# Kernel tuning notes

Measured on AMD Instinct MI355X. Metric: run time of the kernel, lower is better.

The kernel has to match this reference:

```python
import jax, jax.numpy as jnp
import numpy as np

N_EMBD = 1024
N_HEAD = 16
SEQ_LEN = 2048
BATCH = 4
ROPE_THETA = 10000.0


def _rope_tables(T, hd, dtype=jnp.float32):
    freqs = 1.0 / (ROPE_THETA ** (jnp.arange(0, hd, 2, dtype=jnp.float32) / hd))
    t = jnp.arange(T, dtype=jnp.float32)
    ang = jnp.outer(t, freqs)  # [T, hd//2]
    return jnp.cos(ang).astype(dtype), jnp.sin(ang).astype(dtype)


def _apply_rope(x, cos, sin):
    # x: [B,H,T,hd]; cos/sin: [T, hd//2]
    hd = x.shape[-1]
    x1, x2 = x[..., : hd // 2], x[..., hd // 2 :]
    c = cos[None, None, : x.shape[2], :]
    s = sin[None, None, : x.shape[2], :]
    return jnp.concatenate([x1 * c - x2 * s, x2 * c + x1 * s], axis=-1)


def _rms_norm(x):
    eps = jnp.finfo(x.dtype).eps
    return x * jax.lax.rsqrt(jnp.mean(jnp.square(x), axis=-1, keepdims=True) + eps)


def setup_inputs() -> dict:
    key = jax.random.key(0)
    k1, k2, k3, k4 = jax.random.split(key, 4)
    C = N_EMBD
    x = jax.random.normal(k1, (BATCH, SEQ_LEN, C), dtype=jnp.float32)
    w_attn = jax.random.normal(k2, (C, 3 * C), dtype=jnp.float32) * (1.0 / np.sqrt(C))
    w_proj = jax.random.normal(k3, (C, C), dtype=jnp.float32) * (1.0 / np.sqrt(C))
    val_embed = jax.random.normal(k4, (SEQ_LEN, C), dtype=jnp.float32) * 0.02
    return {"x": x, "w_attn": w_attn, "w_proj": w_proj, "val_embed": val_embed}


def reference(x, w_attn, w_proj, val_embed):
    B, T, C = x.shape
    H = N_HEAD
    hd = C // H

    qkv = x @ w_attn  # [B,T,3C]
    q, k, v = jnp.split(qkv, 3, axis=-1)
    v = v + val_embed[:T]

    def to_heads(t):
        return t.reshape(B, T, H, hd).transpose(0, 2, 1, 3)  # [B,H,T,hd]

    q, k, v = to_heads(q), to_heads(k), to_heads(v)

    cos, sin = _rope_tables(T, hd, x.dtype)
    q = _rms_norm(_apply_rope(q, cos, sin))
    k = _rms_norm(_apply_rope(k, cos, sin))

    scale = 1.0 / np.sqrt(hd)
    scores = jnp.einsum("bhqd,bhkd->bhqk", q, k) * scale  # [B,H,T,T]
    causal = jnp.tril(jnp.ones((T, T), dtype=bool))
    scores = jnp.where(causal[None, None], scores, jnp.finfo(scores.dtype).min)
    attn = jax.nn.softmax(scores, axis=-1)
    y = jnp.einsum("bhqk,bhkd->bhqd", attn, v)  # [B,H,T,hd]
    y = y.transpose(0, 2, 1, 3).reshape(B, T, C)
    return y @ w_proj
```

## Files before the change

kernel.cpp:

```cpp
#include <hip/hip_runtime.h>
#include <float.h>
#include <math.h>

#define BB 4
#define TT 2048
#define CC 1024
#define HH 16
#define HD 64
#define C3 3072

typedef __bf16 bf16;
typedef __bf16 bf16x8 __attribute__((ext_vector_type(8)));
typedef __bf16 bf16x4 __attribute__((ext_vector_type(4)));
typedef float f32x4 __attribute__((ext_vector_type(4)));
typedef float f32x16 __attribute__((ext_vector_type(16)));
typedef unsigned int uint32x4 __attribute__((ext_vector_type(4)));

#define QSCALE 0.18033688f

__device__ __forceinline__ void gload16(const void* g, void* l) {
    __builtin_amdgcn_global_load_lds(
        (const __attribute__((address_space(1))) void*)g,
        (__attribute__((address_space(3))) void*)l, 16, 0, 0);
}

__global__ __launch_bounds__(256) void rope_table_k(float* __restrict__ tab) {
    int idx = blockIdx.x * 256 + threadIdx.x;
    if (idx >= TT * 32) return;
    int t = idx >> 5;
    int j = idx & 31;
    float freq = powf(10000.0f, -((float)(2 * j)) / 64.0f);
    float ang = (float)t * freq;
    tab[idx] = cosf(ang);
    tab[TT * 32 + idx] = sinf(ang);
}

__global__ __launch_bounds__(256) void cvt_f2b_k(const float* __restrict__ in,
                                                 bf16* __restrict__ out, int n8) {
    int i = blockIdx.x * 256 + threadIdx.x;
    if (i >= n8) return;
    const float4* p = (const float4*)(in + (size_t)i * 8);
    float4 a = p[0], b = p[1];
    bf16x8 o;
    o[0] = (bf16)a.x; o[1] = (bf16)a.y; o[2] = (bf16)a.z; o[3] = (bf16)a.w;
    o[4] = (bf16)b.x; o[5] = (bf16)b.y; o[6] = (bf16)b.z; o[7] = (bf16)b.w;
    *(bf16x8*)(out + (size_t)i * 8) = o;
}

__global__ __launch_bounds__(256) void transW_k(const float* __restrict__ in,
                                                bf16* __restrict__ out, int K, int N) {
    __shared__ bf16 tile[64][72];
    int n0 = blockIdx.x * 64, k0 = blockIdx.y * 64;
    int t = threadIdx.x;
    int r = t >> 2, c4 = (t & 3) * 16;
    const float4* src = (const float4*)(in + (size_t)(k0 + r) * N + n0 + c4);
    #pragma unroll
    for (int j = 0; j < 4; ++j) {
        float4 v = src[j];
        tile[r][c4 + 4 * j + 0] = (bf16)v.x; tile[r][c4 + 4 * j + 1] = (bf16)v.y;
        tile[r][c4 + 4 * j + 2] = (bf16)v.z; tile[r][c4 + 4 * j + 3] = (bf16)v.w;
    }
    __syncthreads();
    bf16x8 o0, o1;
    #pragma unroll
    for (int j = 0; j < 8; ++j) o0[j] = tile[c4 + j][r];
    #pragma unroll
    for (int j = 0; j < 8; ++j) o1[j] = tile[c4 + 8 + j][r];
    *(bf16x8*)(out + (size_t)(n0 + r) * K + k0 + c4) = o0;
    *(bf16x8*)(out + (size_t)(n0 + r) * K + k0 + c4 + 8) = o1;
}

__global__ __launch_bounds__(512, 1) void gemm256_k(const bf16* __restrict__ A,
                                                    const bf16* __restrict__ BT,
                                                    bf16* __restrict__ Qh,
                                                    bf16* __restrict__ Kh,
                                                    bf16* __restrict__ Vh,
                                                    int M, int N, int K) {
    extern __shared__ bf16 smem[];
    const int tid = threadIdx.x;
    const int w = tid >> 6, lane = tid & 63;
    const int wm = w >> 2, wn = w & 3;
    const int nwg = (int)gridDim.x;
    const int cpx = nwg >> 3;
    const int flat = (int)blockIdx.x;
    const int wg = (flat & 7) * cpx + (flat >> 3);
    const int gx = N / 192;
    const int n0 = (wg % gx) * 192;
    const int m0 = (wg / gx) * 256;

    const int srow = lane >> 3;
    const int schunk = (lane & 7) ^ srow;
    const int xorL = (lane & 7) << 3;
    const int KT = K >> 6;

    const bf16* Bb = BT + (size_t)(n0 + wn * 48 + (lane & 15)) * K + (lane >> 4) * 8;

    f32x4 acc[8][3];
    #pragma unroll
    for (int i = 0; i < 8; ++i)
        #pragma unroll
        for (int j = 0; j < 3; ++j) acc[i][j] = {0.f, 0.f, 0.f, 0.f};

    auto stageA = [&](int kt, bf16* Abuf) {
        const int k0 = kt * 64;
        #pragma unroll
        for (int ri = 0; ri < 4; ++ri) {
            int row = ri * 64 + w * 8;
            gload16(A + (size_t)(m0 + row + srow) * K + k0 + schunk * 8,
                    Abuf + row * 64);
        }
    };

    stageA(0, smem);
    __syncthreads();

    for (int kt = 0; kt < KT; ++kt) {
        const int buf = kt & 1;
        if (kt + 1 < KT) stageA(kt + 1, smem + (buf ^ 1) * 16384);
        const bf16* Al = smem + buf * 16384;
        #pragma unroll
        for (int kh = 0; kh < 2; ++kh) {
            const int off = (kh * 32 + (lane >> 4) * 8) ^ xorL;
            bf16x8 aF[8], bF[3];
            #pragma unroll
            for (int j = 0; j < 3; ++j)
                bF[j] = *(const bf16x8*)(Bb + (size_t)(j * 16) * K + kt * 64 + kh * 32);
            #pragma unroll
            for (int i = 0; i < 8; ++i)
                aF[i] = *(const bf16x8*)&Al[(wm * 128 + i * 16 + (lane & 15)) * 64 + off];
            __builtin_amdgcn_s_setprio(1);
            #pragma unroll
            for (int i = 0; i < 8; ++i)
                #pragma unroll
                for (int j = 0; j < 3; ++j)
                    acc[i][j] = __builtin_amdgcn_mfma_f32_16x16x32_bf16(
                        aF[i], bF[j], acc[i][j], 0, 0, 0);
            __builtin_amdgcn_s_setprio(0);
        }
        __syncthreads();
    }

    const int ncb = n0 + wn * 48;
    #pragma unroll
    for (int j = 0; j < 3; ++j) {
        const int ncbj = ncb + j * 16;
        const int region = ncbj >> 10;
        const int hj = (ncbj & 1023) >> 6;
        const int cj = (ncbj & 63) + (lane & 15);
        bf16* dst = (region == 0) ? Qh : ((region == 1) ? Kh : Vh);
        #pragma unroll
        for (int i = 0; i < 8; ++i)
            #pragma unroll
            for (int r = 0; r < 4; ++r) {
                int m = m0 + wm * 128 + i * 16 + 4 * (lane >> 4) + r;
                int b = m >> 11, t = m & (TT - 1);
                dst[((size_t)(b * HH + hj) * TT + t) * HD + cj] = (bf16)acc[i][j][r];
            }
    }
}

__global__ __launch_bounds__(256) void gemm_bt_k(const bf16* __restrict__ A,
                                                 const bf16* __restrict__ BT,
                                                 float* __restrict__ C,
                                                 int M, int N, int K) {
    __shared__ bf16 Al[128 * 64];
    __shared__ bf16 Bl[128 * 64];
    const int tid = threadIdx.x;
    const int w = tid >> 6, lane = tid & 63;
    const int flat = (int)blockIdx.x;
    const int xcd = flat & 7;
    const int local = flat >> 3;
    const int lr = local >> 3, lc = local & 7;
    const int m0 = (xcd * 8 + lr) * 128;
    const int n0 = lc * 128;
    const int wrow = (w >> 1) * 64, wcol = (w & 1) * 64;
    const int srow = lane >> 3;
    const int selem = (((lane & 7) ^ srow) << 3);
    const int xorL = (lane & 7) << 3;

    const f32x4 fz = {0.f, 0.f, 0.f, 0.f};
    f32x4 acc[4][4];
    #pragma unroll
    for (int i = 0; i < 4; ++i)
        #pragma unroll
        for (int j = 0; j < 4; ++j) acc[i][j] = fz;

    for (int k0 = 0; k0 < K; k0 += 64) {
        __syncthreads();
        #pragma unroll
        for (int jj = 0; jj < 4; ++jj) {
            int c = w * 4 + jj;
            int row = c * 8 + srow;
            gload16(A + (size_t)(m0 + row) * K + k0 + selem, &Al[c * 512]);
            gload16(BT + (size_t)(n0 + row) * K + k0 + selem, &Bl[c * 512]);
        }
        __syncthreads();
        #pragma unroll
        for (int kh = 0; kh < 2; ++kh) {
            const int off = (kh * 32 + (lane >> 4) * 8) ^ xorL;
            bf16x8 aF[4], bF[4];
            #pragma unroll
            for (int i = 0; i < 4; ++i) {
                aF[i] = *(const bf16x8*)&Al[(wrow + i * 16 + (lane & 15)) * 64 + off];
                bF[i] = *(const bf16x8*)&Bl[(wcol + i * 16 + (lane & 15)) * 64 + off];
            }
            #pragma unroll
            for (int i = 0; i < 4; ++i)
                #pragma unroll
                for (int j = 0; j < 4; ++j)
                    acc[i][j] = __builtin_amdgcn_mfma_f32_16x16x32_bf16(
                        aF[i], bF[j], acc[i][j], 0, 0, 0);
        }
    }

    #pragma unroll
    for (int i = 0; i < 4; ++i)
        #pragma unroll
        for (int r = 0; r < 4; ++r) {
            size_t rowm = (size_t)(m0 + wrow + i * 16 + 4 * (lane >> 4) + r);
            #pragma unroll
            for (int j = 0; j < 4; ++j)
                C[rowm * N + n0 + wcol + j * 16 + (lane & 15)] = acc[i][j][r];
        }
}

__global__ __launch_bounds__(256) void rope_rms_k(bf16* __restrict__ Qh,
                                                  bf16* __restrict__ Kh,
                                                  const bf16* __restrict__ Vh,
                                                  bf16* __restrict__ Vt,
                                                  const float* __restrict__ emb,
                                                  const float* __restrict__ tab) {
    __shared__ bf16 tile[64][72];
    const int t0 = blockIdx.x * 64;
    const int bh = blockIdx.y;
    const int h = bh & (HH - 1);
    const int w = threadIdx.x >> 6, lane = threadIdx.x & 63;
    const int j = lane & 31;
    #pragma unroll 4
    for (int i = 0; i < 16; ++i) {
        const int tl = w * 16 + i;
        const int t = t0 + tl;
        const size_t base = ((size_t)bh * TT + t) * HD + lane;
        const float cs = tab[t * 32 + j];
        const float sn = tab[TT * 32 + t * 32 + j];
        float q = (float)Qh[base], k = (float)Kh[base], v = (float)Vh[base];
        float qp = __shfl_xor(q, 32, 64), kp = __shfl_xor(k, 32, 64);
        float rq = (lane < 32) ? q * cs - qp * sn : q * cs + qp * sn;
        float rk = (lane < 32) ? k * cs - kp * sn : k * cs + kp * sn;
        float sq = rq * rq, sk = rk * rk;
        #pragma unroll
        for (int off = 1; off < 64; off <<= 1) {
            sq += __shfl_xor(sq, off, 64);
            sk += __shfl_xor(sk, off, 64);
        }
        rq *= rsqrtf(sq * (1.0f / 64.0f) + 1.1920929e-07f);
        rk *= rsqrtf(sk * (1.0f / 64.0f) + 1.1920929e-07f);
        Qh[base] = (bf16)(rq * QSCALE);
        Kh[base] = (bf16)rk;
        tile[tl][lane] = (bf16)(v + emb[(size_t)t * CC + h * HD + lane]);
    }
    __syncthreads();
    const int tt = threadIdx.x;
    const int r = tt >> 2, c4 = (tt & 3) * 16;
    bf16x8 o0, o1;
    #pragma unroll
    for (int jj = 0; jj < 8; ++jj) o0[jj] = tile[c4 + jj][r];
    #pragma unroll
    for (int jj = 0; jj < 8; ++jj) o1[jj] = tile[c4 + 8 + jj][r];
    bf16* out = Vt + (size_t)bh * HD * TT;
    *(bf16x8*)(out + (size_t)r * TT + t0 + c4) = o0;
    *(bf16x8*)(out + (size_t)r * TT + t0 + c4 + 8) = o1;
}

__global__ __launch_bounds__(512) void attn_k(const bf16* __restrict__ Qh,
                                              const bf16* __restrict__ Kh,
                                              const bf16* __restrict__ Vt,
                                              bf16* __restrict__ Y) {
    extern __shared__ bf16 asmem[];
    bf16* KlB = asmem;
    bf16* VlB = asmem + 16384;
    const int flat = (int)blockIdx.y * 8 + (int)blockIdx.x;
    const int slot = flat >> 3;
    const int bh = (flat & 7) * 8 + (slot & 7);
    const int u = slot >> 3;
    const int qb = (u < 4) ? (7 - u) : (u - 4);
    const int b = bh >> 4, h = bh & 15;
    const int tid = threadIdx.x, w = tid >> 6, lane = tid & 63;
    const int hi = lane >> 5, q31 = lane & 31;
    const int wq0 = qb * 256 + w * 32;
    const int qg = wq0 + q31;
    const int xr = q31 & 7;

    const bf16* Kbase = Kh + (size_t)bh * TT * HD;
    const bf16* Vbase = Vt + (size_t)bh * HD * TT;

    bf16x8 qF[4];
    {
        const bf16* qp = Qh + (size_t)bh * TT * HD + (size_t)qg * HD + hi * 8;
        #pragma unroll
        for (int ds = 0; ds < 4; ++ds) qF[ds] = *(const bf16x8*)(qp + ds * 16);
    }

    f32x16 accY[2];
    #pragma unroll
    for (int i = 0; i < 16; ++i) { accY[0][i] = 0.f; accY[1][i] = 0.f; }
    float mR = -INFINITY, lR = 0.f;

    const int srow = lane >> 3;
    const int schunk = (lane & 7) ^ srow;
    const int vsr = lane >> 4;
    const int ktN = 2 * qb + 2;

    auto stageKV = [&](int kt, int buf) {
        const int kc0 = kt * 128;
        #pragma unroll
        for (int jj = 0; jj < 2; ++jj) {
            int lr = w * 16 + jj * 8;
            gload16(Kbase + (size_t)(kc0 + lr + srow) * HD + schunk * 8,
                    KlB + buf * 8192 + lr * 64);
            int vr = w * 8 + jj * 4;
            int vrow = vr + vsr;
            gload16(Vbase + (size_t)vrow * TT + kc0 + (((lane & 15) ^ (vrow & 7)) * 8),
                    VlB + buf * 8192 + vr * 128);
        }
    };

    stageKV(0, 0);
    asm volatile("s_waitcnt vmcnt(0)" ::: "memory");
    __builtin_amdgcn_s_barrier();
    __builtin_amdgcn_sched_barrier(0);

    for (int kt = 0; kt < ktN; ++kt) {
        const int buf = kt & 1;
        if (kt + 1 < ktN) stageKV(kt + 1, buf ^ 1);
        const bf16* KL = KlB + buf * 8192;
        const bf16* VL = VlB + buf * 8192;
        #pragma unroll
        for (int s = 0; s < 2; ++s) {
            if (kt * 128 + s * 64 > wq0 + 31) break;
            f32x16 sa[2];
            #pragma unroll
            for (int i = 0; i < 16; ++i) { sa[0][i] = 0.f; sa[1][i] = 0.f; }
            __builtin_amdgcn_s_setprio(1);
            #pragma unroll
            for (int ds = 0; ds < 4; ++ds) {
                int cc = ds * 2 + hi;
                bf16x8 k0 = *(const bf16x8*)&KL[(s * 64 + q31) * 64 + ((cc ^ xr) * 8)];
                bf16x8 k1 = *(const bf16x8*)&KL[(s * 64 + 32 + q31) * 64 + ((cc ^ xr) * 8)];
                sa[0] = __builtin_amdgcn_mfma_f32_32x32x16_bf16(k0, qF[ds], sa[0], 0, 0, 0);
                sa[1] = __builtin_amdgcn_mfma_f32_32x32x16_bf16(k1, qF[ds], sa[1], 0, 0, 0);
            }
            __builtin_amdgcn_s_setprio(0);
            if (kt * 128 + s * 64 + 63 > wq0) {
                #pragma unroll
                for (int kb = 0; kb < 2; ++kb)
                    #pragma unroll
                    for (int r = 0; r < 16; ++r) {
                        int k = kt * 128 + s * 64 + kb * 32 + (r & 3) + 8 * (r >> 2) + 4 * hi;
                        if (k > qg) sa[kb][r] = -1e30f;
                    }
            }
            float mx = -1e30f;
            #pragma unroll
            for (int r = 0; r < 16; ++r)
                mx = fmaxf(fmaxf(sa[0][r], sa[1][r]), mx);
            mx = fmaxf(mx, __shfl_xor(mx, 32, 64));
            if (!__all(mx - mR <= 12.0f)) {
                float mnew = fmaxf(mR, mx);
                float alpha = __builtin_amdgcn_exp2f(mR - mnew);
                #pragma unroll
                for (int i = 0; i < 16; ++i) { accY[0][i] *= alpha; accY[1][i] *= alpha; }
                lR *= alpha;
                mR = mnew;
            }
            float sum0 = 0.f, sum1 = 0.f;
            #pragma unroll
            for (int r = 0; r < 16; ++r) {
                float p0 = __builtin_amdgcn_exp2f(sa[0][r] - mR);
                float p1 = __builtin_amdgcn_exp2f(sa[1][r] - mR);
                sa[0][r] = p0; sa[1][r] = p1;
                sum0 += p0; sum1 += p1;
            }
            float sum = sum0 + sum1;
            sum += __shfl_xor(sum, 32, 64);
            lR += sum;
            unsigned int wds[2][8];
            #pragma unroll
            for (int kb = 0; kb < 2; ++kb)
                #pragma unroll
                for (int jj = 0; jj < 8; ++jj) {
                    bf16x8 tmp;
                    tmp[0] = (bf16)sa[kb][2 * jj];
                    tmp[1] = (bf16)sa[kb][2 * jj + 1];
                    wds[kb][jj] = *(unsigned int*)&tmp;
                }
            bf16x8 pF[4];
            #pragma unroll
            for (int ks = 0; ks < 4; ++ks) {
                const int kb = ks >> 1, ss = ks & 1;
                unsigned int w0 = wds[kb][4 * ss + 0], w1 = wds[kb][4 * ss + 1];
                unsigned int w2 = wds[kb][4 * ss + 2], w3 = wds[kb][4 * ss + 3];
                unsigned int t0 = hi ? w0 : w2, t1 = hi ? w1 : w3;
                unsigned int r0 = (unsigned int)__shfl_xor((int)t0, 32, 64);
                unsigned int r1 = (unsigned int)__shfl_xor((int)t1, 32, 64);
                uint32x4 fw;
                fw[0] = hi ? r0 : w0; fw[1] = hi ? r1 : w1;
                fw[2] = hi ? w2 : r0; fw[3] = hi ? w3 : r1;
                pF[ks] = *(bf16x8*)&fw;
            }
            __builtin_amdgcn_s_setprio(1);
            #pragma unroll
            for (int cd = 0; cd < 2; ++cd) {
                const int rowD = cd * 32 + q31;
                #pragma unroll
                for (int ks = 0; ks < 4; ++ks) {
                    int cc = s * 8 + ks * 2 + hi;
                    bf16x8 vA = *(const bf16x8*)&VL[rowD * 128 + ((cc ^ xr) * 8)];
                    accY[cd] = __builtin_amdgcn_mfma_f32_32x32x16_bf16(
                        vA, pF[ks], accY[cd], 0, 0, 0);
                }
            }
            __builtin_amdgcn_s_setprio(0);
        }
        if (kt + 1 < ktN) {
            asm volatile("s_waitcnt vmcnt(0)" ::: "memory");
            __builtin_amdgcn_s_barrier();
            __builtin_amdgcn_sched_barrier(0);
        }
    }

    float inv = 1.0f / lR;
    bf16* yp = Y + ((size_t)(b * TT + qg)) * CC + h * HD;
    #pragma unroll
    for (int cd = 0; cd < 2; ++cd)
        #pragma unroll
        for (int g = 0; g < 4; ++g) {
            int d0 = cd * 32 + 8 * g + 4 * hi;
            bf16x4 o;
            o[0] = (bf16)(accY[cd][4 * g + 0] * inv);
            o[1] = (bf16)(accY[cd][4 * g + 1] * inv);
            o[2] = (bf16)(accY[cd][4 * g + 2] * inv);
            o[3] = (bf16)(accY[cd][4 * g + 3] * inv);
            *(bf16x4*)(yp + d0) = o;
        }
}

extern "C" void kernel_launch(void* const* d_in, const int* in_sizes, int n_in,
                              void* d_out, int out_size, void* d_ws, size_t ws_size,
                              hipStream_t stream) {
    const float* x         = (const float*)d_in[0];
    const float* w_attn    = (const float*)d_in[1];
    const float* w_proj    = (const float*)d_in[2];
    const float* val_embed = (const float*)d_in[3];
    float* out = (float*)d_out;

    bf16* xb  = (bf16*)d_ws;
    bf16* waT = xb + (size_t)8192 * 1024;
    bf16* wpT = waT + (size_t)3072 * 1024;
    bf16* Qh  = wpT + (size_t)1024 * 1024;
    bf16* Kh  = Qh + (size_t)64 * 2048 * 64;
    bf16* Vh  = Kh + (size_t)64 * 2048 * 64;
    bf16* Vt  = Vh + (size_t)64 * 2048 * 64;
    bf16* Yb  = Vt + (size_t)64 * 2048 * 64;
    float* tab = (float*)(Yb + (size_t)64 * 2048 * 64);

    hipFuncSetAttribute((const void*)gemm256_k,
                        hipFuncAttributeMaxDynamicSharedMemorySize, 65536);
    hipFuncSetAttribute((const void*)attn_k,
                        hipFuncAttributeMaxDynamicSharedMemorySize, 65536);

    rope_table_k<<<dim3((TT * 32 + 255) / 256), dim3(256), 0, stream>>>(tab);
    cvt_f2b_k<<<dim3(8192 * 1024 / 8 / 256), dim3(256), 0, stream>>>(x, xb, 8192 * 1024 / 8);
    transW_k<<<dim3(3072 / 64, 1024 / 64), dim3(256), 0, stream>>>(w_attn, waT, 1024, 3072);
    transW_k<<<dim3(1024 / 64, 1024 / 64), dim3(256), 0, stream>>>(w_proj, wpT, 1024, 1024);
    gemm256_k<<<dim3((8192 / 256) * (3072 / 192)), dim3(512), 65536, stream>>>(
        xb, waT, Qh, Kh, Vh, 8192, 3072, 1024);
    rope_rms_k<<<dim3(TT / 64, BB * HH), dim3(256), 0, stream>>>(
        Qh, Kh, Vh, Vt, val_embed, tab);
    attn_k<<<dim3(8, BB * HH), dim3(512), 65536, stream>>>(Qh, Kh, Vt, Yb);
    gemm_bt_k<<<dim3(512), dim3(256), 0, stream>>>(
        Yb, wpT, out, 8192, 1024, 1024);
}
```

Baseline: 208.3 us.

## Stage GEMM B operand through LDS and deepen K/A prefetch pipelines

In the QKV GEMM, the B (weight) tile is now loaded asynchronously into LDS with global_load_lds instead of read directly from global memory into registers. A is triple-buffered with a two-tile lookahead, and partial vmcnt waits replace full syncs. The attention kernel gets the same treatment: K is triple-buffered two tiles ahead and V double-buffered, with a partial vmcnt wait. The aim is to hide global latency better, at the cost of more LDS (144KB for the GEMM, 80KB for attention), which may reduce occupancy.

```diff
diff --git a/kernel.cpp b/kernel.cpp
--- a/kernel.cpp
+++ b/kernel.cpp
@@ -93,15 +93,14 @@
     const int xorL = (lane & 7) << 3;
     const int KT = K >> 6;
 
-    const bf16* Bb = BT + (size_t)(n0 + wn * 48 + (lane & 15)) * K + (lane >> 4) * 8;
-
     f32x4 acc[8][3];
     #pragma unroll
     for (int i = 0; i < 8; ++i)
         #pragma unroll
         for (int j = 0; j < 3; ++j) acc[i][j] = {0.f, 0.f, 0.f, 0.f};
 
-    auto stageA = [&](int kt, bf16* Abuf) {
+    auto stageA = [&](int kt) {
+        bf16* Abuf = smem + (kt % 3) * 16384;
         const int k0 = kt * 64;
         #pragma unroll
         for (int ri = 0; ri < 4; ++ri) {
@@ -110,24 +109,39 @@
                     Abuf + row * 64);
         }
     };
-
-    stageA(0, smem);
-    __syncthreads();
+    auto stageB = [&](int kt) {
+        bf16* Bbuf = smem + 49152 + (kt & 1) * 12288;
+        const int k0 = kt * 64;
+        #pragma unroll
+        for (int ri = 0; ri < 3; ++ri) {
+            int row = ri * 64 + w * 8;
+            gload16(BT + (size_t)(n0 + row + srow) * K + k0 + schunk * 8,
+                    Bbuf + row * 64);
+        }
+    };
+
+    stageA(0);
+    stageB(0);
+    stageA(1);
+    asm volatile("s_waitcnt vmcnt(4)" ::: "memory");
+    __builtin_amdgcn_s_barrier();
+    __builtin_amdgcn_sched_barrier(0);
 
     for (int kt = 0; kt < KT; ++kt) {
-        const int buf = kt & 1;
-        if (kt + 1 < KT) stageA(kt + 1, smem + (buf ^ 1) * 16384);
-        const bf16* Al = smem + buf * 16384;
+        if (kt + 1 < KT) stageB(kt + 1);
+        if (kt + 2 < KT) stageA(kt + 2);
+        const bf16* Al = smem + (kt % 3) * 16384;
+        const bf16* Bl = smem + 49152 + (kt & 1) * 12288;
         #pragma unroll
         for (int kh = 0; kh < 2; ++kh) {
             const int off = (kh * 32 + (lane >> 4) * 8) ^ xorL;
             bf16x8 aF[8], bF[3];
             #pragma unroll
-            for (int j = 0; j < 3; ++j)
-                bF[j] = *(const bf16x8*)(Bb + (size_t)(j * 16) * K + kt * 64 + kh * 32);
-            #pragma unroll
             for (int i = 0; i < 8; ++i)
                 aF[i] = *(const bf16x8*)&Al[(wm * 128 + i * 16 + (lane & 15)) * 64 + off];
+            #pragma unroll
+            for (int j = 0; j < 3; ++j)
+                bF[j] = *(const bf16x8*)&Bl[(wn * 48 + j * 16 + (lane & 15)) * 64 + off];
             __builtin_amdgcn_s_setprio(1);
             #pragma unroll
             for (int i = 0; i < 8; ++i)
@@ -137,7 +151,15 @@
                         aF[i], bF[j], acc[i][j], 0, 0, 0);
             __builtin_amdgcn_s_setprio(0);
         }
-        __syncthreads();
+        if (kt + 1 < KT) {
+            if (kt + 2 < KT) {
+                asm volatile("s_waitcnt vmcnt(4)" ::: "memory");
+            } else {
+                asm volatile("s_waitcnt vmcnt(0)" ::: "memory");
+            }
+            __builtin_amdgcn_s_barrier();
+            __builtin_amdgcn_sched_barrier(0);
+        }
     }
 
     const int ncb = n0 + wn * 48;
@@ -277,8 +299,6 @@
                                               const bf16* __restrict__ Vt,
                                               bf16* __restrict__ Y) {
     extern __shared__ bf16 asmem[];
-    bf16* KlB = asmem;
-    bf16* VlB = asmem + 16384;
     const int flat = (int)blockIdx.y * 8 + (int)blockIdx.x;
     const int slot = flat >> 3;
     const int bh = (flat & 7) * 8 + (slot & 7);
@@ -311,30 +331,40 @@
     const int vsr = lane >> 4;
     const int ktN = 2 * qb + 2;
 
-    auto stageKV = [&](int kt, int buf) {
+    auto stageK = [&](int kt) {
+        bf16* dst = asmem + (kt % 3) * 8192;
         const int kc0 = kt * 128;
         #pragma unroll
         for (int jj = 0; jj < 2; ++jj) {
             int lr = w * 16 + jj * 8;
             gload16(Kbase + (size_t)(kc0 + lr + srow) * HD + schunk * 8,
-                    KlB + buf * 8192 + lr * 64);
+                    dst + lr * 64);
+        }
+    };
+    auto stageV = [&](int kt) {
+        bf16* dst = asmem + 24576 + (kt & 1) * 8192;
+        const int kc0 = kt * 128;
+        #pragma unroll
+        for (int jj = 0; jj < 2; ++jj) {
             int vr = w * 8 + jj * 4;
             int vrow = vr + vsr;
             gload16(Vbase + (size_t)vrow * TT + kc0 + (((lane & 15) ^ (vrow & 7)) * 8),
-                    VlB + buf * 8192 + vr * 128);
+                    dst + vr * 128);
         }
     };
 
-    stageKV(0, 0);
-    asm volatile("s_waitcnt vmcnt(0)" ::: "memory");
+    stageK(0);
+    stageV(0);
+    stageK(1);
+    asm volatile("s_waitcnt vmcnt(2)" ::: "memory");
     __builtin_amdgcn_s_barrier();
     __builtin_amdgcn_sched_barrier(0);
 
     for (int kt = 0; kt < ktN; ++kt) {
-        const int buf = kt & 1;
-        if (kt + 1 < ktN) stageKV(kt + 1, buf ^ 1);
-        const bf16* KL = KlB + buf * 8192;
-        const bf16* VL = VlB + buf * 8192;
+        if (kt + 1 < ktN) stageV(kt + 1);
+        if (kt + 2 < ktN) stageK(kt + 2);
+        const bf16* KL = asmem + (kt % 3) * 8192;
+        const bf16* VL = asmem + 24576 + (kt & 1) * 8192;
         #pragma unroll
         for (int s = 0; s < 2; ++s) {
             if (kt * 128 + s * 64 > wq0 + 31) break;
@@ -423,7 +453,11 @@
             __builtin_amdgcn_s_setprio(0);
         }
         if (kt + 1 < ktN) {
-            asm volatile("s_waitcnt vmcnt(0)" ::: "memory");
+            if (kt + 2 < ktN) {
+                asm volatile("s_waitcnt vmcnt(2)" ::: "memory");
+            } else {
+                asm volatile("s_waitcnt vmcnt(0)" ::: "memory");
+            }
             __builtin_amdgcn_s_barrier();
             __builtin_amdgcn_sched_barrier(0);
         }
@@ -465,19 +499,19 @@
     float* tab = (float*)(Yb + (size_t)64 * 2048 * 64);
 
     hipFuncSetAttribute((const void*)gemm256_k,
-                        hipFuncAttributeMaxDynamicSharedMemorySize, 65536);
+                        hipFuncAttributeMaxDynamicSharedMemorySize, 147456);
     hipFuncSetAttribute((const void*)attn_k,
-                        hipFuncAttributeMaxDynamicSharedMemorySize, 65536);
+                        hipFuncAttributeMaxDynamicSharedMemorySize, 81920);
 
     rope_table_k<<<dim3((TT * 32 + 255) / 256), dim3(256), 0, stream>>>(tab);
     cvt_f2b_k<<<dim3(8192 * 1024 / 8 / 256), dim3(256), 0, stream>>>(x, xb, 8192 * 1024 / 8);
     transW_k<<<dim3(3072 / 64, 1024 / 64), dim3(256), 0, stream>>>(w_attn, waT, 1024, 3072);
     transW_k<<<dim3(1024 / 64, 1024 / 64), dim3(256), 0, stream>>>(w_proj, wpT, 1024, 1024);
-    gemm256_k<<<dim3((8192 / 256) * (3072 / 192)), dim3(512), 65536, stream>>>(
+    gemm256_k<<<dim3((8192 / 256) * (3072 / 192)), dim3(512), 147456, stream>>>(
         xb, waT, Qh, Kh, Vh, 8192, 3072, 1024);
     rope_rms_k<<<dim3(TT / 64, BB * HH), dim3(256), 0, stream>>>(
         Qh, Kh, Vh, Vt, val_embed, tab);
-    attn_k<<<dim3(8, BB * HH), dim3(512), 65536, stream>>>(Qh, Kh, Vt, Yb);
+    attn_k<<<dim3(8, BB * HH), dim3(512), 81920, stream>>>(Qh, Kh, Vt, Yb);
     gemm_bt_k<<<dim3(512), dim3(256), 0, stream>>>(
         Yb, wpT, out, 8192, 1024, 1024);
 }
```

After: 179.4 us. 1.16x faster.
